# Kernel optimization log

Hardware: AMD Instinct MI355X
Metric: run time of the kernel (lower is better)

Reference implementation:

```python
import jax, jax.numpy as jnp
import numpy as np

B, S, D = 4, 2048, 768
H = 12
HD = D // H  # 64
EPS = 1e-12  # F.normalize eps


def setup_inputs() -> dict:
    key = jax.random.key(0)
    ks = jax.random.split(key, 6)
    scale = 1.0 / np.sqrt(D)
    x = jax.random.normal(ks[0], (B, S, D), dtype=jnp.float32)
    Wq = jax.random.normal(ks[1], (D, D), dtype=jnp.float32) * scale
    Wk = jax.random.normal(ks[2], (D, D), dtype=jnp.float32) * scale
    Wv = jax.random.normal(ks[3], (D, D), dtype=jnp.float32) * scale
    Wo = jax.random.normal(ks[4], (D, D), dtype=jnp.float32) * scale
    temperature = jnp.ones((H, 1, 1), dtype=jnp.float32)
    return {"x": x, "Wq": Wq, "Wk": Wk, "Wv": Wv, "Wo": Wo, "temperature": temperature}


def _heads(t):
    # [B,S,D] -> [B,H,S,HD]
    return t.reshape(B, S, H, HD).transpose(0, 2, 1, 3)


def reference(x, Wq, Wk, Wv, Wo, temperature):
    # Linear weights stored torch-style [out,in]: y = x @ W.T
    q = _heads(x @ Wq.T)
    k = _heads(x @ Wk.T)
    v = _heads(x @ Wv.T)
    # cosine-sim normalize (F.normalize: x / max(||x||, eps))
    q = q / jnp.maximum(jnp.linalg.norm(q, axis=-1, keepdims=True), EPS)
    k = k / jnp.maximum(jnp.linalg.norm(k, axis=-1, keepdims=True), EPS)
    # [B,H,S,S] scores with per-head learnable temperature
    attn = jnp.einsum("bhqd,bhkd->bhqk", q, k) * temperature  # temperature broadcasts [H,1,1]
    causal = jnp.tril(jnp.ones((S, S), dtype=bool))
    attn = jnp.where(causal, attn, -jnp.inf)
    attn = jax.nn.softmax(attn, axis=-1)
    out = jnp.einsum("bhqk,bhkd->bhqd", attn, v)
    out = out.transpose(0, 2, 1, 3).reshape(B, S, D)
    return out @ Wo.T
```

## Files before the change

### kernel.cpp

```cpp
#include <hip/hip_runtime.h>
#include <hip/hip_bf16.h>

#define B_ 4
#define S_ 2048
#define D_ 768
#define H_ 12
#define HD_ 64
#define M_ (B_*S_)
#define LOG2E 1.44269504088896f

typedef __attribute__((ext_vector_type(8))) short bf8;
typedef __attribute__((ext_vector_type(4))) float f4;
typedef unsigned short u16;
typedef unsigned int   u32;

typedef __attribute__((address_space(3))) u32 lds_u32;
typedef __attribute__((address_space(1))) const u32 glob_u32;

__device__ __forceinline__ float bf2f(u16 u) {
  union { u32 i; float f; } c; c.i = ((u32)u) << 16; return c.f;
}
__device__ __forceinline__ u16 f2bf(float x) {
  union { float f; u32 i; } c; c.f = x;
  u32 r = (c.i + 0x7FFFu + ((c.i >> 16) & 1u)) >> 16;
  return (u16)r;
}
__device__ __forceinline__ u16 cvt_bf16(float x) {
  u32 r;
  asm("v_cvt_pk_bf16_f32 %0, %1, %1" : "=v"(r) : "v"(x));
  return (u16)r;
}
__device__ __forceinline__ float exp2_raw(float x) {
  float r;
  asm("v_exp_f32 %0, %1" : "=v"(r) : "v"(x));
  return r;
}
__device__ __forceinline__ void glds16(const u16* g, u16* l) {
  __builtin_amdgcn_global_load_lds((glob_u32*)g, (lds_u32*)l, 16, 0, 0);
}

__global__ __launch_bounds__(256) void stage_all(const float* __restrict__ x,
                                                 const float* __restrict__ w0, const float* __restrict__ w1,
                                                 const float* __restrict__ w2, const float* __restrict__ w3,
                                                 u16* __restrict__ xo,
                                                 u16* __restrict__ o0, u16* __restrict__ o1,
                                                 u16* __restrict__ o2, u16* __restrict__ o3,
                                                 int nx4, int nw4)
{
  int y = blockIdx.y;
  const float* src = (y == 0) ? x : (y == 1) ? w0 : (y == 2) ? w1 : (y == 3) ? w2 : w3;
  u16*         dst = (y == 0) ? xo : (y == 1) ? o0 : (y == 2) ? o1 : (y == 3) ? o2 : o3;
  int n4 = (y == 0) ? nx4 : nw4;
  for (int i = blockIdx.x * blockDim.x + threadIdx.x; i < n4; i += gridDim.x * blockDim.x) {
    float4 v = ((const float4*)src)[i];
    ushort4 o;
    o.x = f2bf(v.x); o.y = f2bf(v.y); o.z = f2bf(v.z); o.w = f2bf(v.w);
    ((ushort4*)dst)[i] = o;
  }
}

__global__ __launch_bounds__(256) void stage_cvt(const float* __restrict__ in,
                                                 u16* __restrict__ out, int n4)
{
  for (int i = blockIdx.x * blockDim.x + threadIdx.x; i < n4; i += gridDim.x * blockDim.x) {
    float4 v = ((const float4*)in)[i];
    ushort4 o;
    o.x = f2bf(v.x); o.y = f2bf(v.y); o.z = f2bf(v.z); o.w = f2bf(v.w);
    ((ushort4*)out)[i] = o;
  }
}

__device__ __forceinline__ bf8 ldcvt8(const float* __restrict__ p) {
  float4 a = *(const float4*)p;
  float4 b = *(const float4*)(p + 4);
  bf8 r;
  r[0] = f2bf(a.x); r[1] = f2bf(a.y); r[2] = f2bf(a.z); r[3] = f2bf(a.w);
  r[4] = f2bf(b.x); r[5] = f2bf(b.y); r[6] = f2bf(b.z); r[7] = f2bf(b.w);
  return r;
}

#define MFMA_BF16 __builtin_amdgcn_mfma_f32_16x16x32_bf16

template <int EPI>
__device__ __forceinline__ void gemm_core(u16* lds, int row0, int col0,
                                          const u16* __restrict__ A,
                                          const u16* __restrict__ W,
                                          u16* __restrict__ Cb,
                                          float* __restrict__ Cf,
                                          const float* __restrict__ temp)
{
  u16* a_lds = lds;
  u16* b_lds = lds + 64 * 64;

  const int w  = threadIdx.x >> 6;
  const int ln = threadIdx.x & 63;
  const int li = ln & 15, g = ln >> 4;
  const int wr = w >> 1, wc = w & 1;

  const int srow = ln >> 3;
  const int scol = ((ln & 7) ^ srow) * 8;
  const u16* Abase = A + (size_t)(row0 + srow) * 768 + scol;
  const u16* Bbase = W + (size_t)(col0 + srow) * 768 + scol;

  f4 acc[2][4];
#pragma unroll
  for (int i = 0; i < 2; ++i)
#pragma unroll
    for (int j = 0; j < 4; ++j) acc[i][j] = (f4){0.f, 0.f, 0.f, 0.f};

  for (int kt = 0; kt < 12; ++kt) {
    const int k0 = kt * 64;
#pragma unroll
    for (int i = 0; i < 2; ++i) {
      int seg = w * 2 + i;
      glds16(Abase + (size_t)(seg * 8) * 768 + k0, a_lds + seg * 512);
    }
#pragma unroll
    for (int i = 0; i < 4; ++i) {
      int seg = w * 4 + i;
      glds16(Bbase + (size_t)(seg * 8) * 768 + k0, b_lds + seg * 512);
    }
    asm volatile("s_waitcnt vmcnt(0)" ::: "memory");
    __syncthreads();

#pragma unroll
    for (int kk = 0; kk < 2; ++kk) {
      const int co = (((kk * 4 + g) ^ (li & 7)) * 8);
      bf8 a0 = *(const bf8*)(a_lds + (wr * 32 + li) * 64 + co);
      bf8 a1 = *(const bf8*)(a_lds + (wr * 32 + 16 + li) * 64 + co);
      bf8 b0 = *(const bf8*)(b_lds + (wc * 64 + li) * 64 + co);
      bf8 b1 = *(const bf8*)(b_lds + (wc * 64 + 16 + li) * 64 + co);
      bf8 b2 = *(const bf8*)(b_lds + (wc * 64 + 32 + li) * 64 + co);
      bf8 b3 = *(const bf8*)(b_lds + (wc * 64 + 48 + li) * 64 + co);
      acc[0][0] = MFMA_BF16(a0, b0, acc[0][0], 0, 0, 0);
      acc[0][1] = MFMA_BF16(a0, b1, acc[0][1], 0, 0, 0);
      acc[0][2] = MFMA_BF16(a0, b2, acc[0][2], 0, 0, 0);
      acc[0][3] = MFMA_BF16(a0, b3, acc[0][3], 0, 0, 0);
      acc[1][0] = MFMA_BF16(a1, b0, acc[1][0], 0, 0, 0);
      acc[1][1] = MFMA_BF16(a1, b1, acc[1][1], 0, 0, 0);
      acc[1][2] = MFMA_BF16(a1, b2, acc[1][2], 0, 0, 0);
      acc[1][3] = MFMA_BF16(a1, b3, acc[1][3], 0, 0, 0);
    }
    __syncthreads();
  }

  const int wrow0 = row0 + wr * 32;
  const int wcol0 = col0 + wc * 64;

  if (EPI == 1 || EPI == 2) {
    float tmul = 1.0f;
    if (EPI == 2) tmul = temp[wcol0 >> 6] * LOG2E;
#pragma unroll
    for (int i = 0; i < 2; ++i)
#pragma unroll
      for (int r = 0; r < 4; ++r) {
        float ss = 0.f;
#pragma unroll
        for (int j = 0; j < 4; ++j) ss += acc[i][j][r] * acc[i][j][r];
#pragma unroll
        for (int msk = 1; msk < 16; msk <<= 1) ss += __shfl_xor(ss, msk, 64);
        float scl = tmul / fmaxf(sqrtf(ss), 1e-12f);
#pragma unroll
        for (int j = 0; j < 4; ++j) acc[i][j][r] *= scl;
      }
  }

  if (EPI == 4) {
    __syncthreads();
#pragma unroll
    for (int i = 0; i < 2; ++i)
#pragma unroll
      for (int j = 0; j < 4; ++j)
#pragma unroll
        for (int r = 0; r < 4; ++r) {
          int cl = wc * 64 + j * 16 + li;
          int rl = wr * 32 + i * 16 + g * 4 + r;
          lds[cl * 64 + rl] = cvt_bf16(acc[i][j][r]);
        }
    __syncthreads();
    const int sb = row0 & 2047;
    const int bb = row0 >> 11;
#pragma unroll
    for (int q = 0; q < 4; ++q) {
      int c2 = threadIdx.x * 4 + q;
      int cl = c2 >> 3;
      int s8 = (c2 & 7) * 8;
      int colg = col0 + cl;
      int bh = bb * H_ + (colg >> 6);
      int d  = colg & 63;
      *(bf8*)(Cb + ((size_t)bh * 64 + d) * 2048 + sb + s8) = *(const bf8*)&lds[cl * 64 + s8];
    }
    return;
  }

#pragma unroll
  for (int i = 0; i < 2; ++i)
#pragma unroll
    for (int j = 0; j < 4; ++j)
#pragma unroll
      for (int r = 0; r < 4; ++r) {
        int row = wrow0 + i * 16 + g * 4 + r;
        int col = wcol0 + j * 16 + li;
        if (EPI == 3) Cf[(size_t)row * 768 + col] = acc[i][j][r];
        else          Cb[(size_t)row * 768 + col] = f2bf(acc[i][j][r]);
      }
}

__global__ __launch_bounds__(256) void gemm_qkv(const u16* __restrict__ XB,
                                                const u16* __restrict__ Wq, const u16* __restrict__ Wk,
                                                const u16* __restrict__ Wv,
                                                u16* __restrict__ Qb, u16* __restrict__ Kb,
                                                u16* __restrict__ Vt,
                                                const float* __restrict__ temp)
{
  __shared__ __align__(16) u16 lds[192 * 64];
  const int bid  = blockIdx.x;
  const int xcd  = bid & 7;
  const int j    = bid >> 3;
  const int row0 = (xcd * 16 + j / 18) * 64;
  const int rest = j % 18;
  const int z    = rest / 6;
  const int col0 = (rest % 6) * 128;
  if (z == 0)      gemm_core<2>(lds, row0, col0, XB, Wq, Qb, nullptr, temp);
  else if (z == 1) gemm_core<1>(lds, row0, col0, XB, Wk, Kb, nullptr, temp);
  else             gemm_core<4>(lds, row0, col0, XB, Wv, Vt, nullptr, temp);
}

__global__ __launch_bounds__(256) void gemm_out(const u16* __restrict__ A,
                                                const u16* __restrict__ W,
                                                float* __restrict__ Cf)
{
  __shared__ __align__(16) u16 lds[192 * 64];
  const int bid  = blockIdx.x;
  const int xcd  = bid & 7;
  const int j    = bid >> 3;
  const int row0 = (xcd * 16 + j / 6) * 64;
  const int col0 = (j % 6) * 128;
  gemm_core<3>(lds, row0, col0, A, W, nullptr, Cf, nullptr);
}

template <int EPI>
__global__ __launch_bounds__(256) void gemm_wf32(const u16* __restrict__ A,
                                                 const float* __restrict__ W,
                                                 u16* __restrict__ Cb,
                                                 float* __restrict__ Cf,
                                                 const float* __restrict__ temp)
{
  const int w  = threadIdx.x >> 6;
  const int ln = threadIdx.x & 63;
  const int li = ln & 15, g = ln >> 4;
  const int wr = w >> 1, wc = w & 1;
  const int row0 = blockIdx.x * 64 + wr * 32;
  const int col0 = blockIdx.y * 128 + wc * 64;

  const u16*   Ap = A + (size_t)(row0 + li) * 768 + g * 8;
  const float* Wp = W + (size_t)(col0 + li) * 768 + g * 8;

  f4 acc[2][4];
#pragma unroll
  for (int i = 0; i < 2; ++i)
#pragma unroll
    for (int j = 0; j < 4; ++j) acc[i][j] = (f4){0.f, 0.f, 0.f, 0.f};

  for (int k = 0; k < 768; k += 32) {
    bf8 a0 = *(const bf8*)(Ap + k);
    bf8 a1 = *(const bf8*)(Ap + (size_t)16 * 768 + k);
    bf8 b0 = ldcvt8(Wp + k);
    bf8 b1 = ldcvt8(Wp + (size_t)16 * 768 + k);
    bf8 b2 = ldcvt8(Wp + (size_t)32 * 768 + k);
    bf8 b3 = ldcvt8(Wp + (size_t)48 * 768 + k);
    acc[0][0] = MFMA_BF16(a0, b0, acc[0][0], 0, 0, 0);
    acc[0][1] = MFMA_BF16(a0, b1, acc[0][1], 0, 0, 0);
    acc[0][2] = MFMA_BF16(a0, b2, acc[0][2], 0, 0, 0);
    acc[0][3] = MFMA_BF16(a0, b3, acc[0][3], 0, 0, 0);
    acc[1][0] = MFMA_BF16(a1, b0, acc[1][0], 0, 0, 0);
    acc[1][1] = MFMA_BF16(a1, b1, acc[1][1], 0, 0, 0);
    acc[1][2] = MFMA_BF16(a1, b2, acc[1][2], 0, 0, 0);
    acc[1][3] = MFMA_BF16(a1, b3, acc[1][3], 0, 0, 0);
  }

  if (EPI == 1 || EPI == 2) {
    float tmul = 1.0f;
    if (EPI == 2) tmul = temp[col0 >> 6] * LOG2E;
#pragma unroll
    for (int i = 0; i < 2; ++i)
#pragma unroll
      for (int r = 0; r < 4; ++r) {
        float ss = 0.f;
#pragma unroll
        for (int j = 0; j < 4; ++j) ss += acc[i][j][r] * acc[i][j][r];
#pragma unroll
        for (int msk = 1; msk < 16; msk <<= 1) ss += __shfl_xor(ss, msk, 64);
        float scl = tmul / fmaxf(sqrtf(ss), 1e-12f);
#pragma unroll
        for (int j = 0; j < 4; ++j) acc[i][j][r] *= scl;
      }
  }

#pragma unroll
  for (int i = 0; i < 2; ++i)
#pragma unroll
    for (int j = 0; j < 4; ++j)
#pragma unroll
      for (int r = 0; r < 4; ++r) {
        int row = row0 + i * 16 + g * 4 + r;
        int col = col0 + j * 16 + li;
        if (EPI == 3)      Cf[(size_t)row * 768 + col] = acc[i][j][r];
        else if (EPI == 0) Cb[((size_t)((row >> 11) * H_ + (col >> 6)) * 64 + (col & 63)) * 2048
                              + (row & 2047)] = f2bf(acc[i][j][r]);
        else               Cb[(size_t)row * 768 + col] = f2bf(acc[i][j][r]);
      }
}

__global__ __launch_bounds__(256, 4) void flash_attn(const u16* __restrict__ Q,
                                                     const u16* __restrict__ K,
                                                     const u16* __restrict__ Vt,
                                                     u16* __restrict__ O,
                                                     const float* __restrict__ temp)
{
  const int bid = blockIdx.x;
  const int xcd = bid & 7;
  const int j   = bid >> 3;
  const int bh  = xcd * 6 + j % 6;
  const int qt  = 31 - j / 6;
  const int b = bh / H_, h = bh % H_;
  const size_t base = (size_t)b * S_ * D_ + h * HD_;
  const u16* Qp  = Q + base;
  const u16* Kp  = K + base;
  const u16* Vtp = Vt + (size_t)bh * 64 * 2048;
  u16*       Op  = O + base;

  const float C2 = fabsf(temp[h]) * LOG2E;

  const int w  = threadIdx.x >> 6;
  const int ln = threadIdx.x & 63;
  const int li = ln & 15, g = ln >> 4;

  __shared__ __align__(16) u16 k_lds[64][72];
  __shared__ __align__(16) u16 vt[64][72];
  __shared__ __align__(16) u16 p_lds[4][16][72];

  const int q0 = qt * 64;
  const int qrow = q0 + w * 16 + li;

  bf8 qf0 = *(const bf8*)(Qp + (size_t)qrow * D_ + g * 8);
  bf8 qf1 = *(const bf8*)(Qp + (size_t)qrow * D_ + 32 + g * 8);

  const int r2 = (threadIdx.x >> 3) * 2;
  const int c0 = (threadIdx.x & 7) * 8;
  const u16* ksrc = Kp  + (size_t)r2 * D_ + c0;
  const u16* vsrc = Vtp + (size_t)r2 * 2048 + c0;

  bf8 ka = *(const bf8*)(ksrc);
  bf8 kb = *(const bf8*)(ksrc + D_);
  bf8 va = *(const bf8*)(vsrc);
  bf8 vb_ = *(const bf8*)(vsrc + 2048);

  f4 o[4];
  float lp[4] = {0.f, 0.f, 0.f, 0.f};
#pragma unroll
  for (int c = 0; c < 4; ++c) o[c] = (f4){0.f, 0.f, 0.f, 0.f};

  for (int kt = 0; kt <= qt; ++kt) {
    __syncthreads();
    {
      *(bf8*)&k_lds[r2][c0]     = ka;
      *(bf8*)&k_lds[r2 + 1][c0] = kb;
      *(bf8*)&vt[r2][c0]        = va;
      *(bf8*)&vt[r2 + 1][c0]    = vb_;
    }
    if (kt < qt) {
      const u16* ks = ksrc + (size_t)(kt + 1) * 64 * D_;
      const u16* vs = vsrc + (kt + 1) * 64;
      ka  = *(const bf8*)(ks);
      kb  = *(const bf8*)(ks + D_);
      va  = *(const bf8*)(vs);
      vb_ = *(const bf8*)(vs + 2048);
    }
    asm volatile("s_waitcnt lgkmcnt(0)" ::: "memory");
    __builtin_amdgcn_s_barrier();

    f4 sc[4];
#pragma unroll
    for (int c = 0; c < 4; ++c) sc[c] = (f4){0.f, 0.f, 0.f, 0.f};
#pragma unroll
    for (int c = 0; c < 4; ++c) {
      bf8 k0 = *(const bf8*)&k_lds[c * 16 + li][g * 8];
      bf8 k1 = *(const bf8*)&k_lds[c * 16 + li][32 + g * 8];
      sc[c] = MFMA_BF16(qf0, k0, sc[c], 0, 0, 0);
      sc[c] = MFMA_BF16(qf1, k1, sc[c], 0, 0, 0);
    }

    if (kt == qt) {
#pragma unroll
      for (int c = 0; c < 4; ++c)
#pragma unroll
        for (int r = 0; r < 4; ++r) {
          int col = kt * 64 + c * 16 + li;
          int row = q0 + w * 16 + g * 4 + r;
          if (col > row) sc[c][r] = -__builtin_inff();
        }
    }

#pragma unroll
    for (int c = 0; c < 4; ++c)
#pragma unroll
      for (int r = 0; r < 4; ++r) {
        float p = exp2_raw(sc[c][r] - C2);
        sc[c][r] = p;
        lp[r] += p;
      }

#pragma unroll
    for (int c = 0; c < 4; ++c)
#pragma unroll
      for (int r = 0; r < 4; ++r)
        p_lds[w][g * 4 + r][(c * 16 + li) ^ (g << 3)] = cvt_bf16(sc[c][r]);

#pragma unroll
    for (int ks = 0; ks < 2; ++ks) {
      bf8 pa = *(const bf8*)&p_lds[w][li][(ks * 32 + g * 8) ^ ((li >> 2) << 3)];
#pragma unroll
      for (int c = 0; c < 4; ++c) {
        bf8 vv = *(const bf8*)&vt[c * 16 + li][ks * 32 + g * 8];
        o[c] = MFMA_BF16(pa, vv, o[c], 0, 0, 0);
      }
    }
  }

  float l[4];
#pragma unroll
  for (int r = 0; r < 4; ++r) {
    float s = lp[r];
#pragma unroll
    for (int msk = 1; msk < 16; msk <<= 1) s += __shfl_xor(s, msk, 64);
    l[r] = 1.0f / s;
  }
#pragma unroll
  for (int c = 0; c < 4; ++c)
#pragma unroll
    for (int r = 0; r < 4; ++r) {
      int row = q0 + w * 16 + g * 4 + r;
      Op[(size_t)row * D_ + c * 16 + li] = cvt_bf16(o[c][r] * l[r]);
    }
}

extern "C" void kernel_launch(void* const* d_in, const int* in_sizes, int n_in,
                              void* d_out, int out_size, void* d_ws, size_t ws_size,
                              hipStream_t stream) {
  const void *xv, *Wqv, *Wkv, *Wvv, *Wov, *tv;
  if (in_sizes[0] == M_ * D_) {
    xv = d_in[0]; Wqv = d_in[1]; Wkv = d_in[2]; Wvv = d_in[3]; Wov = d_in[4]; tv = d_in[5];
  } else {
    Wkv = d_in[0]; Wov = d_in[1]; Wqv = d_in[2]; Wvv = d_in[3]; tv = d_in[4]; xv = d_in[5];
  }
  const float* x    = (const float*)xv;
  const float* Wq   = (const float*)Wqv;
  const float* Wk   = (const float*)Wkv;
  const float* Wv   = (const float*)Wvv;
  const float* Wo   = (const float*)Wov;
  const float* temp = (const float*)tv;

  const size_t SZ  = (size_t)M_ * D_;
  const size_t WSZ = (size_t)D_ * D_;
  u16* ws = (u16*)d_ws;
  u16* Qb = ws;
  u16* Kb = ws + SZ;
  u16* Vt = ws + 2 * SZ;
  u16* XB = (u16*)d_out;

  const bool stageW = ws_size >= (3 * SZ + 4 * WSZ) * sizeof(u16);
  u16* Wqb = ws + 3 * SZ;
  u16* Wkb = Wqb + WSZ;
  u16* Wvb = Wkb + WSZ;
  u16* Wob = Wvb + WSZ;

  if (stageW) {
    stage_all<<<dim3(512, 5), 256, 0, stream>>>(x, Wq, Wk, Wv, Wo,
                                                XB, Wqb, Wkb, Wvb, Wob,
                                                (int)(SZ / 4), (int)(WSZ / 4));
    gemm_qkv<<<2304, 256, 0, stream>>>(XB, Wqb, Wkb, Wvb, Qb, Kb, Vt, temp);
    flash_attn<<<1536, 256, 0, stream>>>(Qb, Kb, Vt, Qb, temp);
    gemm_out<<<768, 256, 0, stream>>>(Qb, Wob, (float*)d_out);
  } else {
    dim3 gg(M_ / 64, D_ / 128), bb(256);
    stage_cvt<<<2048, 256, 0, stream>>>(x, XB, (int)(SZ / 4));
    gemm_wf32<2><<<gg, bb, 0, stream>>>(XB, Wq, Qb, nullptr, temp);
    gemm_wf32<1><<<gg, bb, 0, stream>>>(XB, Wk, Kb, nullptr, temp);
    gemm_wf32<0><<<gg, bb, 0, stream>>>(XB, Wv, Vt, nullptr, temp);
    flash_attn<<<1536, 256, 0, stream>>>(Qb, Kb, Vt, Qb, temp);
    gemm_wf32<3><<<gg, bb, 0, stream>>>(Qb, Wo, nullptr, (float*)d_out, temp);
  }
}
```

Measured before the change: 130.5 us.

## Process 128 query rows per flash-attention block, 32 per wave

Each flash-attention block now covers a 128-row query tile instead of 64, with every wave computing two 16-row sub-tiles against the same K/V tile held in LDS. This halves the number of K/V tile loads and LDS staging rounds per query row, and each LDS K/V fragment read now feeds twice as many MFMAs. In exchange, the grid shrinks to 768 blocks and register pressure rises (launch bounds drop from 4 to 3 blocks per CU). The coarser causal tiles also make work across blocks more uneven.

Result: faster. 126.8 us (-2.8%).

```diff
diff --git a/kernel.cpp b/kernel.cpp
--- a/kernel.cpp
+++ b/kernel.cpp
@@ -312,7 +312,7 @@
       }
 }
 
-__global__ __launch_bounds__(256, 4) void flash_attn(const u16* __restrict__ Q,
+__global__ __launch_bounds__(256, 3) void flash_attn(const u16* __restrict__ Q,
                                                      const u16* __restrict__ K,
                                                      const u16* __restrict__ Vt,
                                                      u16* __restrict__ O,
@@ -322,7 +322,7 @@
   const int xcd = bid & 7;
   const int j   = bid >> 3;
   const int bh  = xcd * 6 + j % 6;
-  const int qt  = 31 - j / 6;
+  const int qt  = 15 - j / 6;
   const int b = bh / H_, h = bh % H_;
   const size_t base = (size_t)b * S_ * D_ + h * HD_;
   const u16* Qp  = Q + base;
@@ -338,13 +338,17 @@
 
   __shared__ __align__(16) u16 k_lds[64][72];
   __shared__ __align__(16) u16 vt[64][72];
-  __shared__ __align__(16) u16 p_lds[4][16][72];
-
-  const int q0 = qt * 64;
-  const int qrow = q0 + w * 16 + li;
-
-  bf8 qf0 = *(const bf8*)(Qp + (size_t)qrow * D_ + g * 8);
-  bf8 qf1 = *(const bf8*)(Qp + (size_t)qrow * D_ + 32 + g * 8);
+  __shared__ __align__(16) u16 p_lds[4][32][72];
+
+  const int q0 = qt * 128;
+
+  bf8 qf[2][2];
+#pragma unroll
+  for (int i = 0; i < 2; ++i) {
+    const u16* qp = Qp + (size_t)(q0 + w * 32 + i * 16 + li) * D_;
+    qf[i][0] = *(const bf8*)(qp + g * 8);
+    qf[i][1] = *(const bf8*)(qp + 32 + g * 8);
+  }
 
   const int r2 = (threadIdx.x >> 3) * 2;
   const int c0 = (threadIdx.x & 7) * 8;
@@ -356,12 +360,15 @@
   bf8 va = *(const bf8*)(vsrc);
   bf8 vb_ = *(const bf8*)(vsrc + 2048);
 
-  f4 o[4];
-  float lp[4] = {0.f, 0.f, 0.f, 0.f};
-#pragma unroll
-  for (int c = 0; c < 4; ++c) o[c] = (f4){0.f, 0.f, 0.f, 0.f};
-
-  for (int kt = 0; kt <= qt; ++kt) {
+  f4 o[2][4];
+  float lp[2][4];
+#pragma unroll
+  for (int i = 0; i < 2; ++i)
+#pragma unroll
+    for (int c = 0; c < 4; ++c) { o[i][c] = (f4){0.f, 0.f, 0.f, 0.f}; lp[i][c] = 0.f; }
+
+  const int nt = 2 * qt + 1;
+  for (int kt = 0; kt <= nt; ++kt) {
     __syncthreads();
     {
       *(bf8*)&k_lds[r2][c0]     = ka;
@@ -369,7 +376,7 @@
       *(bf8*)&vt[r2][c0]        = va;
       *(bf8*)&vt[r2 + 1][c0]    = vb_;
     }
-    if (kt < qt) {
+    if (kt < nt) {
       const u16* ks = ksrc + (size_t)(kt + 1) * 64 * D_;
       const u16* vs = vsrc + (kt + 1) * 64;
       ka  = *(const bf8*)(ks);
@@ -380,69 +387,84 @@
     asm volatile("s_waitcnt lgkmcnt(0)" ::: "memory");
     __builtin_amdgcn_s_barrier();
 
-    f4 sc[4];
-#pragma unroll
-    for (int c = 0; c < 4; ++c) sc[c] = (f4){0.f, 0.f, 0.f, 0.f};
+    f4 sc[2][4];
+#pragma unroll
+    for (int i = 0; i < 2; ++i)
+#pragma unroll
+      for (int c = 0; c < 4; ++c) sc[i][c] = (f4){0.f, 0.f, 0.f, 0.f};
 #pragma unroll
     for (int c = 0; c < 4; ++c) {
       bf8 k0 = *(const bf8*)&k_lds[c * 16 + li][g * 8];
       bf8 k1 = *(const bf8*)&k_lds[c * 16 + li][32 + g * 8];
-      sc[c] = MFMA_BF16(qf0, k0, sc[c], 0, 0, 0);
-      sc[c] = MFMA_BF16(qf1, k1, sc[c], 0, 0, 0);
-    }
-
-    if (kt == qt) {
+      sc[0][c] = MFMA_BF16(qf[0][0], k0, sc[0][c], 0, 0, 0);
+      sc[0][c] = MFMA_BF16(qf[0][1], k1, sc[0][c], 0, 0, 0);
+      sc[1][c] = MFMA_BF16(qf[1][0], k0, sc[1][c], 0, 0, 0);
+      sc[1][c] = MFMA_BF16(qf[1][1], k1, sc[1][c], 0, 0, 0);
+    }
+
+    if (kt >= 2 * qt) {
+#pragma unroll
+      for (int i = 0; i < 2; ++i)
+#pragma unroll
+        for (int c = 0; c < 4; ++c)
+#pragma unroll
+          for (int r = 0; r < 4; ++r) {
+            int col = kt * 64 + c * 16 + li;
+            int row = q0 + w * 32 + i * 16 + g * 4 + r;
+            if (col > row) sc[i][c][r] = -__builtin_inff();
+          }
+    }
+
+#pragma unroll
+    for (int i = 0; i < 2; ++i)
 #pragma unroll
       for (int c = 0; c < 4; ++c)
 #pragma unroll
         for (int r = 0; r < 4; ++r) {
-          int col = kt * 64 + c * 16 + li;
-          int row = q0 + w * 16 + g * 4 + r;
-          if (col > row) sc[c][r] = -__builtin_inff();
+          float p = exp2_raw(sc[i][c][r] - C2);
+          sc[i][c][r] = p;
+          lp[i][r] += p;
         }
-    }
-
-#pragma unroll
-    for (int c = 0; c < 4; ++c)
-#pragma unroll
-      for (int r = 0; r < 4; ++r) {
-        float p = exp2_raw(sc[c][r] - C2);
-        sc[c][r] = p;
-        lp[r] += p;
-      }
-
-#pragma unroll
-    for (int c = 0; c < 4; ++c)
-#pragma unroll
-      for (int r = 0; r < 4; ++r)
-        p_lds[w][g * 4 + r][(c * 16 + li) ^ (g << 3)] = cvt_bf16(sc[c][r]);
+
+#pragma unroll
+    for (int i = 0; i < 2; ++i)
+#pragma unroll
+      for (int c = 0; c < 4; ++c)
+#pragma unroll
+        for (int r = 0; r < 4; ++r)
+          p_lds[w][i * 16 + g * 4 + r][(c * 16 + li) ^ (g << 3)] = cvt_bf16(sc[i][c][r]);
 
 #pragma unroll
     for (int ks = 0; ks < 2; ++ks) {
-      bf8 pa = *(const bf8*)&p_lds[w][li][(ks * 32 + g * 8) ^ ((li >> 2) << 3)];
+      bf8 pa0 = *(const bf8*)&p_lds[w][li][(ks * 32 + g * 8) ^ ((li >> 2) << 3)];
+      bf8 pa1 = *(const bf8*)&p_lds[w][16 + li][(ks * 32 + g * 8) ^ ((li >> 2) << 3)];
 #pragma unroll
       for (int c = 0; c < 4; ++c) {
         bf8 vv = *(const bf8*)&vt[c * 16 + li][ks * 32 + g * 8];
-        o[c] = MFMA_BF16(pa, vv, o[c], 0, 0, 0);
+        o[0][c] = MFMA_BF16(pa0, vv, o[0][c], 0, 0, 0);
+        o[1][c] = MFMA_BF16(pa1, vv, o[1][c], 0, 0, 0);
       }
     }
   }
 
-  float l[4];
-#pragma unroll
-  for (int r = 0; r < 4; ++r) {
-    float s = lp[r];
-#pragma unroll
-    for (int msk = 1; msk < 16; msk <<= 1) s += __shfl_xor(s, msk, 64);
-    l[r] = 1.0f / s;
-  }
-#pragma unroll
-  for (int c = 0; c < 4; ++c)
+#pragma unroll
+  for (int i = 0; i < 2; ++i)
 #pragma unroll
     for (int r = 0; r < 4; ++r) {
-      int row = q0 + w * 16 + g * 4 + r;
-      Op[(size_t)row * D_ + c * 16 + li] = cvt_bf16(o[c][r] * l[r]);
-    }
+      float s = lp[i][r];
+#pragma unroll
+      for (int msk = 1; msk < 16; msk <<= 1) s += __shfl_xor(s, msk, 64);
+      lp[i][r] = 1.0f / s;
+    }
+#pragma unroll
+  for (int i = 0; i < 2; ++i)
+#pragma unroll
+    for (int c = 0; c < 4; ++c)
+#pragma unroll
+      for (int r = 0; r < 4; ++r) {
+        int row = q0 + w * 32 + i * 16 + g * 4 + r;
+        Op[(size_t)row * D_ + c * 16 + li] = cvt_bf16(o[i][c][r] * lp[i][r]);
+      }
 }
 
 extern "C" void kernel_launch(void* const* d_in, const int* in_sizes, int n_in,
@@ -480,7 +502,7 @@
                                                 XB, Wqb, Wkb, Wvb, Wob,
                                                 (int)(SZ / 4), (int)(WSZ / 4));
     gemm_qkv<<<2304, 256, 0, stream>>>(XB, Wqb, Wkb, Wvb, Qb, Kb, Vt, temp);
-    flash_attn<<<1536, 256, 0, stream>>>(Qb, Kb, Vt, Qb, temp);
+    flash_attn<<<768, 256, 0, stream>>>(Qb, Kb, Vt, Qb, temp);
     gemm_out<<<768, 256, 0, stream>>>(Qb, Wob, (float*)d_out);
   } else {
     dim3 gg(M_ / 64, D_ / 128), bb(256);
@@ -488,7 +510,7 @@
     gemm_wf32<2><<<gg, bb, 0, stream>>>(XB, Wq, Qb, nullptr, temp);
     gemm_wf32<1><<<gg, bb, 0, stream>>>(XB, Wk, Kb, nullptr, temp);
     gemm_wf32<0><<<gg, bb, 0, stream>>>(XB, Wv, Vt, nullptr, temp);
-    flash_attn<<<1536, 256, 0, stream>>>(Qb, Kb, Vt, Qb, temp);
+    flash_attn<<<768, 256, 0, stream>>>(Qb, Kb, Vt, Qb, temp);
     gemm_wf32<3><<<gg, bb, 0, stream>>>(Qb, Wo, nullptr, (float*)d_out, temp);
   }
 }
```
